# Optimization experiments

Hardware: AMD Instinct MI355X
Metric: run time of the kernel (lower is better)

Reference implementation:

```python
import jax, jax.numpy as jnp
import numpy as np

EMBED_DIM = 1024
NUM_HEADS = 16
HEAD_DIM = EMBED_DIM // NUM_HEADS


def setup_inputs() -> dict:
    key = jax.random.key(0)
    ks = jax.random.split(key, 5)
    B, T, D = 4, 2048, EMBED_DIM
    s = 1.0 / np.sqrt(D)
    return {
        "x": jax.random.normal(ks[0], (B, T, D), dtype=jnp.float32),
        "qkv_w": jax.random.uniform(ks[1], (3 * D, D), jnp.float32, -s, s),
        "qkv_b": jax.random.uniform(ks[2], (3 * D,), jnp.float32, -s, s),
        "out_w": jax.random.uniform(ks[3], (D, D), jnp.float32, -s, s),
        "out_b": jax.random.uniform(ks[4], (D,), jnp.float32, -s, s),
    }


def reference(x, qkv_w, qkv_b, out_w, out_b):
    B, T, D = x.shape
    H, Hd = NUM_HEADS, HEAD_DIM
    qkv = x @ qkv_w.T + qkv_b                      # [B,T,3D]
    q, k, v = jnp.split(qkv, 3, axis=-1)
    def split_heads(t):
        return t.reshape(B, T, H, Hd).transpose(0, 2, 1, 3)  # [B,H,T,Hd]
    q, k, v = split_heads(q), split_heads(k), split_heads(v)
    scores = jnp.einsum("bhqd,bhkd->bhqk", q, k) / np.sqrt(Hd).astype(jnp.float32)
    w = jax.nn.softmax(scores, axis=-1)
    o = jnp.einsum("bhqk,bhkd->bhqd", w, v)        # [B,H,T,Hd]
    o = o.transpose(0, 2, 1, 3).reshape(B, T, D)
    return o @ out_w.T + out_b
```

## Files before the change

kernel.cpp:

```cpp
#include <hip/hip_runtime.h>
#include <stdint.h>


#define BD   4
#define TD   2048
#define DD   1024
#define HH   16
#define HDD  64
#define MM   8192

typedef __attribute__((ext_vector_type(8))) short  bf16x8;
typedef __attribute__((ext_vector_type(4))) float  f32x4;

typedef const __attribute__((address_space(1))) uint8_t gu8;
typedef __attribute__((address_space(3))) uint8_t       lu8;

__device__ __forceinline__ void async_copy16(const void* g, void* l) {
    __builtin_amdgcn_global_load_lds((gu8*)(uintptr_t)g, (lu8*)(uintptr_t)l, 16, 0, 0);
}

__device__ __forceinline__ ushort f2bf(float f) {
    uint32_t u = __float_as_uint(f);
    u += 0x7fffu + ((u >> 16) & 1u);
    return (ushort)(u >> 16);
}

__device__ __forceinline__ float fexp2(float x) {
#if __has_builtin(__builtin_amdgcn_exp2f)
    return __builtin_amdgcn_exp2f(x);
#else
    return __expf(x * 0.69314718056f);
#endif
}

__global__ __launch_bounds__(256) void castk3(const float* __restrict__ a, ushort* __restrict__ ao, int na4,
                                              const float* __restrict__ b, ushort* __restrict__ bo, int nb4,
                                              const float* __restrict__ c, ushort* __restrict__ co, int nc4) {
    const int stride = gridDim.x * blockDim.x;
    const int t0 = blockIdx.x * blockDim.x + threadIdx.x;
    for (int i = t0; i < na4; i += stride) {
        float4 v = ((const float4*)a)[i];
        ushort4 o; o.x = f2bf(v.x); o.y = f2bf(v.y); o.z = f2bf(v.z); o.w = f2bf(v.w);
        ((ushort4*)ao)[i] = o;
    }
    for (int i = t0; i < nb4; i += stride) {
        float4 v = ((const float4*)b)[i];
        ushort4 o; o.x = f2bf(v.x); o.y = f2bf(v.y); o.z = f2bf(v.z); o.w = f2bf(v.w);
        ((ushort4*)bo)[i] = o;
    }
    for (int i = t0; i < nc4; i += stride) {
        float4 v = ((const float4*)c)[i];
        ushort4 o; o.x = f2bf(v.x); o.y = f2bf(v.y); o.z = f2bf(v.z); o.w = f2bf(v.w);
        ((ushort4*)co)[i] = o;
    }
}

template <int MODE>
__global__ __launch_bounds__(256, 2) void gemm_bt(const ushort* __restrict__ A,
                                                  const ushort* __restrict__ W,
                                                  const float* __restrict__ bias,
                                                  float* __restrict__ outf,
                                                  ushort* __restrict__ qb,
                                                  ushort* __restrict__ kb,
                                                  ushort* __restrict__ vb,
                                                  int N) {
    constexpr int K = 1024;
    __shared__ ushort As[128 * 64];
    __shared__ ushort Bs[128 * 64];

    const int t    = threadIdx.x;
    const int lane = t & 63;
    const int wave = t >> 6;
    const int lg   = lane >> 4;
    const int l16  = lane & 15;
    const int wm   = wave >> 1;
    const int wn   = wave & 1;
    const int m0   = blockIdx.x * 128;
    const int n0   = blockIdx.y * 128;

    const int srow = t >> 3;
    const int scol = (t & 7) * 8;

    f32x4 acc[4][4] = {};

    for (int kt = 0; kt < K / 64; ++kt) {
        const ushort* Agp = A + (size_t)(m0 + srow) * K + kt * 64 + scol;
        const ushort* Wgp = W + (size_t)(n0 + srow) * K + kt * 64 + scol;
#pragma unroll
        for (int i = 0; i < 4; ++i) {
            async_copy16(Agp + (size_t)i * 32 * K, (char*)As + i * 4096 + t * 16);
            async_copy16(Wgp + (size_t)i * 32 * K, (char*)Bs + i * 4096 + t * 16);
        }
        __syncthreads();

#pragma unroll
        for (int kk = 0; kk < 2; ++kk) {
            bf16x8 af[4], bf[4];
#pragma unroll
            for (int m = 0; m < 4; ++m)
                af[m] = *(const bf16x8*)((const char*)As +
                        (wm * 64 + m * 16 + l16) * 128 + kk * 64 + lg * 16);
#pragma unroll
            for (int n = 0; n < 4; ++n)
                bf[n] = *(const bf16x8*)((const char*)Bs +
                        (wn * 64 + n * 16 + l16) * 128 + kk * 64 + lg * 16);
#pragma unroll
            for (int m = 0; m < 4; ++m)
#pragma unroll
                for (int n = 0; n < 4; ++n)
                    acc[m][n] = __builtin_amdgcn_mfma_f32_16x16x32_bf16(
                        af[m], bf[n], acc[m][n], 0, 0, 0);
        }
        __syncthreads();
    }

#pragma unroll
    for (int mf = 0; mf < 4; ++mf) {
#pragma unroll
        for (int nf = 0; nf < 4; ++nf) {
            f32x4 a = acc[mf][nf];
            const int n  = n0 + wn * 64 + nf * 16 + l16;
            const float bv = bias[n];
            if constexpr (MODE == 0) {
                const int which = n >> 10;
                const int dcol  = n & 1023;
                const int h  = dcol >> 6;
                const int hd = dcol & 63;
                const int mrow0 = m0 + wm * 64 + mf * 16 + lg * 4;
                const int b   = mrow0 >> 11;
                const int tt0 = mrow0 & 2047;
                if (which == 0) {
#pragma unroll
                    for (int r = 0; r < 4; ++r)
                        qb[(((size_t)(b * HH + h)) * TD + tt0 + r) * HDD + hd] =
                            f2bf((a[r] + bv) * 0.180336880f);
                } else if (which == 1) {
#pragma unroll
                    for (int r = 0; r < 4; ++r)
                        kb[(((size_t)(b * HH + h)) * TD + tt0 + r) * HDD + hd] =
                            f2bf(a[r] + bv);
                } else {
                    ushort4 pk;
                    pk.x = f2bf(a[0] + bv); pk.y = f2bf(a[1] + bv);
                    pk.z = f2bf(a[2] + bv); pk.w = f2bf(a[3] + bv);
                    *(ushort4*)(&vb[(((size_t)(b * HH + h)) * HDD + hd) * TD + tt0]) = pk;
                }
            } else {
#pragma unroll
                for (int r = 0; r < 4; ++r) {
                    const int m = m0 + wm * 64 + mf * 16 + lg * 4 + r;
                    outf[(size_t)m * N + n] = a[r] + bv;
                }
            }
        }
    }
}

__global__ __launch_bounds__(256, 3) void flash_attn(const ushort* __restrict__ Q,
                                                     const ushort* __restrict__ K,
                                                     const ushort* __restrict__ Vt,
                                                     ushort* __restrict__ O) {
    __shared__ char   Ks[2][8192];
    __shared__ char   Vs[2][8192];
    __shared__ ushort Pl[4][32 * 72];

    const int t    = threadIdx.x;
    const int lane = t & 63;
    const int wave = t >> 6;
    const int lg   = lane >> 4;
    const int l16  = lane & 15;

    const int lin  = blockIdx.y * 16 + blockIdx.x;
    const int work = (lin & 7) * 128 + (lin >> 3);
    const int bh   = work >> 4;
    const int q0   = (work & 15) * 128;

    const size_t base = (size_t)bh * TD * HDD;
    const ushort* Qp = Q  + base;
    const ushort* Kp = K  + base;
    const ushort* Vp = Vt + base;

    bf16x8 qf[2][2];
#pragma unroll
    for (int mf = 0; mf < 2; ++mf)
#pragma unroll
        for (int kk = 0; kk < 2; ++kk)
            qf[mf][kk] = *(const bf16x8*)(Qp +
                (q0 + wave * 32 + mf * 16 + l16) * HDD + kk * 32 + lg * 8);

    bf16x8 vone;
    {
        const short ov = (l16 == 0) ? (short)0x3F80 : (short)0;
        vone = bf16x8{ov, ov, ov, ov, ov, ov, ov, ov};
    }

    f32x4 o[2][4] = {};
    f32x4 osum[2] = {};

    const int sr = t >> 3;
    const int sc = ((t & 7) * 16) ^ ((sr & 7) << 4);
    const int ldst = t * 16;

#define STAGE(buf, kv)                                                         \
    do {                                                                       \
        const char* kg_ = (const char*)(Kp + (size_t)((kv) + sr) * HDD) + sc;  \
        async_copy16(kg_,                 &Ks[buf][0]    + ldst);              \
        async_copy16(kg_ + 32 * HDD * 2,  &Ks[buf][4096] + ldst);              \
        const char* vg_ = (const char*)(Vp + (size_t)sr * TD + (kv)) + sc;     \
        async_copy16(vg_,                 &Vs[buf][0]    + ldst);              \
        async_copy16(vg_ + 32 * TD * 2,   &Vs[buf][4096] + ldst);              \
    } while (0)

    STAGE(0, 0);
    int cur = 0;

    const int kxor = (l16 & 7) << 4;

    for (int kv0 = 0; kv0 < TD; kv0 += 64) {
        STAGE(cur ^ 1, (kv0 + 64) & (TD - 1));

        asm volatile("s_waitcnt vmcnt(4)" ::: "memory");
        asm volatile("s_barrier" ::: "memory");

        bf16x8 kf[2][4], vf[2][4];
#pragma unroll
        for (int kk = 0; kk < 2; ++kk)
#pragma unroll
            for (int nf = 0; nf < 4; ++nf)
                kf[kk][nf] = *(const bf16x8*)(&Ks[cur][(nf * 16 + l16) * 128 +
                                              ((kk * 64 + lg * 16) ^ kxor)]);
#pragma unroll
        for (int kk2 = 0; kk2 < 2; ++kk2)
#pragma unroll
            for (int df = 0; df < 4; ++df)
                vf[kk2][df] = *(const bf16x8*)(&Vs[cur][(df * 16 + l16) * 128 +
                                               ((kk2 * 64 + lg * 16) ^ kxor)]);

        f32x4 s[2][4] = {};
        __builtin_amdgcn_s_setprio(1);
#pragma unroll
        for (int kk = 0; kk < 2; ++kk)
#pragma unroll
            for (int mf = 0; mf < 2; ++mf)
#pragma unroll
                for (int nf = 0; nf < 4; ++nf)
                    s[mf][nf] = __builtin_amdgcn_mfma_f32_16x16x32_bf16(
                        qf[mf][kk], kf[kk][nf], s[mf][nf], 0, 0, 0);
        __builtin_amdgcn_s_setprio(0);

#pragma unroll
        for (int mf = 0; mf < 2; ++mf)
#pragma unroll
            for (int nf = 0; nf < 4; ++nf)
#pragma unroll
                for (int r = 0; r < 4; ++r)
                    Pl[wave][(mf * 16 + lg * 4 + r) * 72 + nf * 16 + l16] =
                        f2bf(fexp2(s[mf][nf][r]));

        __builtin_amdgcn_s_setprio(1);
#pragma unroll
        for (int kk2 = 0; kk2 < 2; ++kk2) {
            bf16x8 pf[2];
#pragma unroll
            for (int mf = 0; mf < 2; ++mf)
                pf[mf] = *(const bf16x8*)(&Pl[wave][(mf * 16 + l16) * 72 +
                                                    kk2 * 32 + lg * 8]);
#pragma unroll
            for (int mf = 0; mf < 2; ++mf) {
#pragma unroll
                for (int df = 0; df < 4; ++df)
                    o[mf][df] = __builtin_amdgcn_mfma_f32_16x16x32_bf16(
                        pf[mf], vf[kk2][df], o[mf][df], 0, 0, 0);
                osum[mf] = __builtin_amdgcn_mfma_f32_16x16x32_bf16(
                        pf[mf], vone, osum[mf], 0, 0, 0);
            }
        }
        __builtin_amdgcn_s_setprio(0);

        asm volatile("s_waitcnt lgkmcnt(0)" ::: "memory");
        __builtin_amdgcn_sched_barrier(0);
        asm volatile("s_barrier" ::: "memory");
        cur ^= 1;
    }
#undef STAGE

    const int b = bh >> 4, h = bh & 15;
#pragma unroll
    for (int mf = 0; mf < 2; ++mf) {
#pragma unroll
        for (int r = 0; r < 4; ++r) {
            const float l   = __shfl(osum[mf][r], lane & 48);
            const float inv = 1.0f / l;
            const int tq = q0 + wave * 32 + mf * 16 + lg * 4 + r;
#pragma unroll
            for (int df = 0; df < 4; ++df)
                O[((size_t)(b * TD + tq)) * DD + h * HDD + df * 16 + l16] =
                    f2bf(o[mf][df][r] * inv);
        }
    }
}

extern "C" void kernel_launch(void* const* d_in, const int* in_sizes, int n_in,
                              void* d_out, int out_size, void* d_ws, size_t ws_size,
                              hipStream_t stream) {
    (void)in_sizes; (void)n_in; (void)out_size; (void)ws_size;

    const float* x     = (const float*)d_in[0];
    const float* qkv_w = (const float*)d_in[1];
    const float* qkv_b = (const float*)d_in[2];
    const float* out_w = (const float*)d_in[3];
    const float* out_b = (const float*)d_in[4];

    char* ws = (char*)d_ws;
    ushort* xb  = (ushort*)(ws);
    ushort* w1b = (ushort*)(ws + (16u << 20));
    ushort* w2b = (ushort*)(ws + (22u << 20));
    ushort* qb  = (ushort*)(ws + (24u << 20));
    ushort* kb  = (ushort*)(ws + (40u << 20));
    ushort* vb  = (ushort*)(ws + (56u << 20));
    ushort* ob  = (ushort*)(ws + (72u << 20));

    castk3<<<2048, 256, 0, stream>>>(x, xb, MM * DD / 4,
                                     qkv_w, w1b, 3 * DD * DD / 4,
                                     out_w, w2b, DD * DD / 4);

    gemm_bt<0><<<dim3(MM / 128, 3 * DD / 128), 256, 0, stream>>>(
        xb, w1b, qkv_b, nullptr, qb, kb, vb, 3 * DD);

    flash_attn<<<dim3(TD / 128, BD * HH), 256, 0, stream>>>(qb, kb, vb, ob);

    gemm_bt<1><<<dim3(MM / 128, DD / 128), 256, 0, stream>>>(
        ob, w2b, out_b, (float*)d_out, nullptr, nullptr, nullptr, DD);
}
```

Measured before the change: 275.7 us.

## Add dedicated 256x256 double-buffered QKV GEMM with swizzled LDS and tile remap

```diff
diff --git a/kernel.cpp b/kernel.cpp
--- a/kernel.cpp
+++ b/kernel.cpp
@@ -55,15 +55,175 @@
     }
 }
 
-template <int MODE>
-__global__ __launch_bounds__(256, 2) void gemm_bt(const ushort* __restrict__ A,
-                                                  const ushort* __restrict__ W,
-                                                  const float* __restrict__ bias,
-                                                  float* __restrict__ outf,
-                                                  ushort* __restrict__ qb,
-                                                  ushort* __restrict__ kb,
-                                                  ushort* __restrict__ vb,
-                                                  int N) {
+__global__ __launch_bounds__(512, 1) void gemm_qkv(const ushort* __restrict__ A,
+                                                   const ushort* __restrict__ W,
+                                                   const float* __restrict__ bias,
+                                                   ushort* __restrict__ qb,
+                                                   ushort* __restrict__ kb,
+                                                   ushort* __restrict__ vb) {
+    constexpr int K = 1024;
+    __shared__ ushort As[2][16384];
+    __shared__ ushort Bs[2][16384];
+
+    const int t    = threadIdx.x;
+    const int lane = t & 63;
+    const int wave = t >> 6;
+    const int lg   = lane >> 4;
+    const int l16  = lane & 15;
+    const int wm   = wave >> 2;
+    const int wn   = wave & 3;
+
+    const int lin  = blockIdx.y * 32 + blockIdx.x;
+    const int work = (lin & 7) * 48 + (lin >> 3);
+    const int m0   = (work & 31) * 256;
+    const int n0   = (work >> 5) * 256;
+
+    const int srow = t >> 3;
+    const int scol = ((t & 7) * 16) ^ ((srow & 7) << 4);
+    const int kxor = (l16 & 7) << 4;
+
+#define STAGE(gbase, lbase, kt)                                                \
+    do {                                                                       \
+        const char* s_ = (const char*)((gbase) + (size_t)srow * K +            \
+                                       (size_t)(kt) * 64) + scol;              \
+        char* d_ = (char*)(lbase) + t * 16;                                    \
+        async_copy16(s_, d_);                                                  \
+        async_copy16(s_ + (size_t)64 * K * 2, d_ + 8192);                      \
+    } while (0)
+
+#define LDA(dst, mf, kk)                                                       \
+    dst = *(const bf16x8*)((const char*)&As[cur][0] +                          \
+          (wm * 128 + (mf) * 16 + l16) * 128 + (((kk) * 64 + lg * 16) ^ kxor))
+#define LDB(dst, nf, kk)                                                       \
+    dst = *(const bf16x8*)((const char*)&Bs[cur][0] +                          \
+          (wn * 64 + (nf) * 16 + l16) * 128 + (((kk) * 64 + lg * 16) ^ kxor))
+
+    f32x4 acc[8][4] = {};
+
+    STAGE(A + (size_t)m0 * K,         &As[0][0],    0);
+    STAGE(A + (size_t)(m0 + 128) * K, &As[0][8192], 0);
+    STAGE(W + (size_t)n0 * K,         &Bs[0][0],    0);
+    STAGE(W + (size_t)(n0 + 128) * K, &Bs[0][8192], 0);
+    asm volatile("s_waitcnt vmcnt(0)" ::: "memory");
+    asm volatile("s_barrier" ::: "memory");
+    __builtin_amdgcn_sched_barrier(0);
+
+    for (int kt = 0; kt < 16; ++kt) {
+        const int cur = kt & 1;
+        const int nb  = cur ^ 1;
+        const int ktn = (kt + 1) & 15;
+        bf16x8 af[4][2], bfr[4][2];
+
+        STAGE(A + (size_t)m0 * K,         &As[nb][0],    ktn);
+        STAGE(A + (size_t)(m0 + 128) * K, &As[nb][8192], ktn);
+#pragma unroll
+        for (int mf = 0; mf < 4; ++mf) { LDA(af[mf][0], mf, 0); LDA(af[mf][1], mf, 1); }
+#pragma unroll
+        for (int nf = 0; nf < 2; ++nf) { LDB(bfr[nf][0], nf, 0); LDB(bfr[nf][1], nf, 1); }
+        asm volatile("s_waitcnt lgkmcnt(0)" ::: "memory");
+        __builtin_amdgcn_sched_barrier(0);
+        __builtin_amdgcn_s_setprio(1);
+#pragma unroll
+        for (int mf = 0; mf < 4; ++mf)
+#pragma unroll
+            for (int nf = 0; nf < 2; ++nf)
+#pragma unroll
+                for (int kk = 0; kk < 2; ++kk)
+                    acc[mf][nf] = __builtin_amdgcn_mfma_f32_16x16x32_bf16(
+                        af[mf][kk], bfr[nf][kk], acc[mf][nf], 0, 0, 0);
+        __builtin_amdgcn_s_setprio(0);
+
+        STAGE(W + (size_t)n0 * K,         &Bs[nb][0],    ktn);
+        STAGE(W + (size_t)(n0 + 128) * K, &Bs[nb][8192], ktn);
+#pragma unroll
+        for (int nf = 2; nf < 4; ++nf) { LDB(bfr[nf][0], nf, 0); LDB(bfr[nf][1], nf, 1); }
+        asm volatile("s_waitcnt lgkmcnt(0)" ::: "memory");
+        __builtin_amdgcn_sched_barrier(0);
+        __builtin_amdgcn_s_setprio(1);
+#pragma unroll
+        for (int mf = 0; mf < 4; ++mf)
+#pragma unroll
+            for (int nf = 2; nf < 4; ++nf)
+#pragma unroll
+                for (int kk = 0; kk < 2; ++kk)
+                    acc[mf][nf] = __builtin_amdgcn_mfma_f32_16x16x32_bf16(
+                        af[mf][kk], bfr[nf][kk], acc[mf][nf], 0, 0, 0);
+        __builtin_amdgcn_s_setprio(0);
+
+#pragma unroll
+        for (int mf = 0; mf < 4; ++mf) { LDA(af[mf][0], mf + 4, 0); LDA(af[mf][1], mf + 4, 1); }
+        asm volatile("s_waitcnt lgkmcnt(0)" ::: "memory");
+        __builtin_amdgcn_sched_barrier(0);
+        __builtin_amdgcn_s_setprio(1);
+#pragma unroll
+        for (int mf = 0; mf < 4; ++mf)
+#pragma unroll
+            for (int nf = 2; nf < 4; ++nf)
+#pragma unroll
+                for (int kk = 0; kk < 2; ++kk)
+                    acc[mf + 4][nf] = __builtin_amdgcn_mfma_f32_16x16x32_bf16(
+                        af[mf][kk], bfr[nf][kk], acc[mf + 4][nf], 0, 0, 0);
+        __builtin_amdgcn_s_setprio(0);
+
+        __builtin_amdgcn_s_setprio(1);
+#pragma unroll
+        for (int mf = 0; mf < 4; ++mf)
+#pragma unroll
+            for (int nf = 0; nf < 2; ++nf)
+#pragma unroll
+                for (int kk = 0; kk < 2; ++kk)
+                    acc[mf + 4][nf] = __builtin_amdgcn_mfma_f32_16x16x32_bf16(
+                        af[mf][kk], bfr[nf][kk], acc[mf + 4][nf], 0, 0, 0);
+        __builtin_amdgcn_s_setprio(0);
+
+        asm volatile("s_waitcnt vmcnt(0)" ::: "memory");
+        __builtin_amdgcn_sched_barrier(0);
+        asm volatile("s_barrier" ::: "memory");
+        __builtin_amdgcn_sched_barrier(0);
+    }
+#undef STAGE
+#undef LDA
+#undef LDB
+
+#pragma unroll
+    for (int mf = 0; mf < 8; ++mf) {
+#pragma unroll
+        for (int nf = 0; nf < 4; ++nf) {
+            f32x4 a = acc[mf][nf];
+            const int n  = n0 + wn * 64 + nf * 16 + l16;
+            const float bv = bias[n];
+            const int which = n >> 10;
+            const int dcol  = n & 1023;
+            const int h  = dcol >> 6;
+            const int hd = dcol & 63;
+            const int mrow0 = m0 + wm * 128 + mf * 16 + lg * 4;
+            const int b   = mrow0 >> 11;
+            const int tt0 = mrow0 & 2047;
+            if (which == 0) {
+#pragma unroll
+                for (int r = 0; r < 4; ++r)
+                    qb[(((size_t)(b * HH + h)) * TD + tt0 + r) * HDD + hd] =
+                        f2bf((a[r] + bv) * 0.180336880f);
+            } else if (which == 1) {
+#pragma unroll
+                for (int r = 0; r < 4; ++r)
+                    kb[(((size_t)(b * HH + h)) * TD + tt0 + r) * HDD + hd] =
+                        f2bf(a[r] + bv);
+            } else {
+                ushort4 pk;
+                pk.x = f2bf(a[0] + bv); pk.y = f2bf(a[1] + bv);
+                pk.z = f2bf(a[2] + bv); pk.w = f2bf(a[3] + bv);
+                *(ushort4*)(&vb[(((size_t)(b * HH + h)) * HDD + hd) * TD + tt0]) = pk;
+            }
+        }
+    }
+}
+
+__global__ __launch_bounds__(256, 2) void gemm_out(const ushort* __restrict__ A,
+                                                   const ushort* __restrict__ W,
+                                                   const float* __restrict__ bias,
+                                                   float* __restrict__ outf,
+                                                   int N) {
     constexpr int K = 1024;
     __shared__ ushort As[128 * 64];
     __shared__ ushort Bs[128 * 64];
@@ -121,36 +281,10 @@
             f32x4 a = acc[mf][nf];
             const int n  = n0 + wn * 64 + nf * 16 + l16;
             const float bv = bias[n];
-            if constexpr (MODE == 0) {
-                const int which = n >> 10;
-                const int dcol  = n & 1023;
-                const int h  = dcol >> 6;
-                const int hd = dcol & 63;
-                const int mrow0 = m0 + wm * 64 + mf * 16 + lg * 4;
-                const int b   = mrow0 >> 11;
-                const int tt0 = mrow0 & 2047;
-                if (which == 0) {
-#pragma unroll
-                    for (int r = 0; r < 4; ++r)
-                        qb[(((size_t)(b * HH + h)) * TD + tt0 + r) * HDD + hd] =
-                            f2bf((a[r] + bv) * 0.180336880f);
-                } else if (which == 1) {
-#pragma unroll
-                    for (int r = 0; r < 4; ++r)
-                        kb[(((size_t)(b * HH + h)) * TD + tt0 + r) * HDD + hd] =
-                            f2bf(a[r] + bv);
-                } else {
-                    ushort4 pk;
-                    pk.x = f2bf(a[0] + bv); pk.y = f2bf(a[1] + bv);
-                    pk.z = f2bf(a[2] + bv); pk.w = f2bf(a[3] + bv);
-                    *(ushort4*)(&vb[(((size_t)(b * HH + h)) * HDD + hd) * TD + tt0]) = pk;
-                }
-            } else {
-#pragma unroll
-                for (int r = 0; r < 4; ++r) {
-                    const int m = m0 + wm * 64 + mf * 16 + lg * 4 + r;
-                    outf[(size_t)m * N + n] = a[r] + bv;
-                }
+#pragma unroll
+            for (int r = 0; r < 4; ++r) {
+                const int m = m0 + wm * 64 + mf * 16 + lg * 4 + r;
+                outf[(size_t)m * N + n] = a[r] + bv;
             }
         }
     }
@@ -324,11 +458,11 @@
                                      qkv_w, w1b, 3 * DD * DD / 4,
                                      out_w, w2b, DD * DD / 4);
 
-    gemm_bt<0><<<dim3(MM / 128, 3 * DD / 128), 256, 0, stream>>>(
-        xb, w1b, qkv_b, nullptr, qb, kb, vb, 3 * DD);
+    gemm_qkv<<<dim3(MM / 256, 3 * DD / 256), 512, 0, stream>>>(
+        xb, w1b, qkv_b, qb, kb, vb);
 
     flash_attn<<<dim3(TD / 128, BD * HH), 256, 0, stream>>>(qb, kb, vb, ob);
 
-    gemm_bt<1><<<dim3(MM / 128, DD / 128), 256, 0, stream>>>(
-        ob, w2b, out_b, (float*)d_out, nullptr, nullptr, nullptr, DD);
-}
+    gemm_out<<<dim3(MM / 128, DD / 128), 256, 0, stream>>>(
+        ob, w2b, out_b, (float*)d_out, DD);
+}
```

Measured after the change: 284.7 us. +3.3%, slower.
